# Kernel optimization log

Hardware: AMD Instinct MI355X
Metric: run time of the kernel (lower is better)

## Reference

```python
import jax, jax.numpy as jnp
import numpy as np

N_NODES = 100000
N_EDGES = 640000
D_IN = 128
D_H = 128


def setup_inputs() -> dict:
    key = jax.random.key(0)
    ks = jax.random.split(key, 24)
    def W(k, shp):
        return jax.random.normal(k, shp, dtype=jnp.float32) * 0.05
    inp = {
        "x": jax.random.normal(ks[0], (N_NODES, D_IN), dtype=jnp.float32),
        "src": jax.random.randint(ks[1], (N_EDGES,), 0, N_NODES, dtype=jnp.int32),
        "dst": jax.random.randint(ks[2], (N_EDGES,), 0, N_NODES, dtype=jnp.int32),
        "neg_src": jax.random.randint(ks[3], (N_EDGES,), 0, N_NODES, dtype=jnp.int32),
        "neg_dst": jax.random.randint(ks[4], (N_EDGES,), 0, N_NODES, dtype=jnp.int32),
        # SAGEConv layer 1/2/3: fc_self weight, fc_neigh weight (stored [in,out]), bias
        "Ws1": W(ks[5], (D_IN, D_H)), "Wn1": W(ks[6], (D_IN, D_H)), "b1": jnp.zeros((D_H,), jnp.float32),
        "Ws2": W(ks[7], (D_H, D_H)), "Wn2": W(ks[8], (D_H, D_H)), "b2": jnp.zeros((D_H,), jnp.float32),
        "Ws3": W(ks[9], (D_H, D_H)), "Wn3": W(ks[10], (D_H, D_H)), "b3": jnp.zeros((D_H,), jnp.float32),
        # MLPPredictor: W1 [2h,h], W2 [h,1]
        "Wp1": W(ks[11], (2 * D_H, D_H)), "bp1": jnp.zeros((D_H,), jnp.float32),
        "Wp2": W(ks[12], (D_H, 1)), "bp2": jnp.zeros((1,), jnp.float32),
    }
    return inp


def _sage_mean(x, src, dst, Ws, Wn, b):
    # DGL SAGEConv 'mean': rst = fc_self(h) + fc_neigh(mean_{in-neighbors}(h)) + bias
    n = x.shape[0]
    msum = jax.ops.segment_sum(x[src], dst, num_segments=n)        # [N, d]
    deg = jax.ops.segment_sum(jnp.ones_like(src, dtype=x.dtype), dst, num_segments=n)
    mean = msum / jnp.clip(deg, 1.0)[:, None]                      # zero for isolated nodes
    return x @ Ws + mean @ Wn + b


def _edge_score(h, s, d, Wp1, bp1, Wp2, bp2):
    z = jnp.concatenate([h[s], h[d]], axis=1)                      # [E, 2h]
    return (jax.nn.relu(z @ Wp1 + bp1) @ Wp2 + bp2)[:, 0]          # [E]


def reference(x, src, dst, neg_src, neg_dst,
              Ws1, Wn1, b1, Ws2, Wn2, b2, Ws3, Wn3, b3,
              Wp1, bp1, Wp2, bp2):
    h = _sage_mean(x, src, dst, Ws1, Wn1, b1)
    h = _sage_mean(h, src, dst, Ws2, Wn2, b2)
    h = _sage_mean(h, src, dst, Ws3, Wn3, b3)
    pos = _edge_score(h, src, dst, Wp1, bp1, Wp2, bp2)
    neg = _edge_score(h, neg_src, neg_dst, Wp1, bp1, Wp2, bp2)
    return (pos, neg)
```

## Files before the change

### kernel.cpp

```cpp
#include <hip/hip_runtime.h>

#define N_NODES 100000
#define N_EDGES 640000
#define D 128
#define SCAN_TILE 1024
#define SCAN_BLOCKS ((N_NODES + SCAN_TILE - 1) / SCAN_TILE)

typedef __attribute__((ext_vector_type(8))) short bf16x8;
typedef __attribute__((ext_vector_type(4))) float f32x4;

__device__ __forceinline__ unsigned short f32_to_bf16(float f) {
  union { float f; unsigned int u; } v; v.f = f;
  unsigned int u = v.u;
  unsigned int r = (u + 0x7fffu + ((u >> 16) & 1u)) >> 16;
  return (unsigned short)r;
}
__device__ __forceinline__ float bf16_lo(unsigned int u) { return __uint_as_float(u << 16); }
__device__ __forceinline__ float bf16_hi(unsigned int u) { return __uint_as_float(u & 0xffff0000u); }

__device__ __forceinline__ void acc8(float* a, uint4 r) {
  a[0] += bf16_lo(r.x); a[1] += bf16_hi(r.x);
  a[2] += bf16_lo(r.y); a[3] += bf16_hi(r.y);
  a[4] += bf16_lo(r.z); a[5] += bf16_hi(r.z);
  a[6] += bf16_lo(r.w); a[7] += bf16_hi(r.w);
}

__global__ void zero_i32(int* __restrict__ p, int n) {
  int i = blockIdx.x * blockDim.x + threadIdx.x;
  if (i < n) p[i] = 0;
}

__global__ void f32_to_bf16_vec(const float* __restrict__ in, unsigned short* __restrict__ out, int n4) {
  int i = blockIdx.x * blockDim.x + threadIdx.x;
  if (i < n4) {
    float4 v = ((const float4*)in)[i];
    ushort4 o;
    o.x = f32_to_bf16(v.x); o.y = f32_to_bf16(v.y);
    o.z = f32_to_bf16(v.z); o.w = f32_to_bf16(v.w);
    ((ushort4*)out)[i] = o;
  }
}

__global__ void transpose_w(const float* __restrict__ W0, const float* __restrict__ W1,
                            const float* __restrict__ W2, const float* __restrict__ W3,
                            const float* __restrict__ W4, const float* __restrict__ W5,
                            const float* __restrict__ W6, const float* __restrict__ W7,
                            unsigned short* __restrict__ wt) {
  int id = blockIdx.x * 256 + threadIdx.x;
  int mat = id >> 14;
  int rem = id & 16383;
  int n = rem >> 7, k = rem & 127;
  const float* Wm = mat < 4 ? (mat < 2 ? (mat == 0 ? W0 : W1) : (mat == 2 ? W2 : W3))
                            : (mat < 6 ? (mat == 4 ? W4 : W5) : (mat == 6 ? W6 : W7));
  wt[id] = f32_to_bf16(Wm[k * D + n]);
}

__global__ void hist_kernel(const int* __restrict__ dst, int* __restrict__ deg, int E) {
  int i = blockIdx.x * blockDim.x + threadIdx.x;
  if (i < E) atomicAdd(&deg[dst[i]], 1);
}

__global__ void scan_blocksum(const int* __restrict__ deg, int* __restrict__ partial, int n) {
  __shared__ int lds[256];
  const int tid = threadIdx.x;
  const int base = blockIdx.x * SCAN_TILE + tid * 4;
  int s = 0;
#pragma unroll
  for (int j = 0; j < 4; ++j) {
    int i = base + j;
    if (i < n) s += deg[i];
  }
  lds[tid] = s;
  __syncthreads();
  for (int off = 128; off > 0; off >>= 1) {
    if (tid < off) lds[tid] += lds[tid + off];
    __syncthreads();
  }
  if (tid == 0) partial[blockIdx.x] = lds[0];
}

__global__ void scan_offsets(int* __restrict__ partial, int* __restrict__ row_start, int nb, int n) {
  __shared__ int lds[128];
  const int tid = threadIdx.x;
  int v = (tid < nb) ? partial[tid] : 0;
  lds[tid] = v;
  __syncthreads();
  for (int off = 1; off < 128; off <<= 1) {
    int t = (tid >= off) ? lds[tid - off] : 0;
    __syncthreads();
    lds[tid] += t;
    __syncthreads();
  }
  if (tid < nb) partial[tid] = (tid == 0) ? 0 : lds[tid - 1];
  if (tid == 0) row_start[n] = lds[nb - 1];
}

__global__ void scan_final(const int* __restrict__ deg, const int* __restrict__ partial,
                           int* __restrict__ row_start, int n) {
  __shared__ int lds[256];
  const int tid = threadIdx.x;
  const int base = blockIdx.x * SCAN_TILE + tid * 4;
  int d[4];
  int s = 0;
#pragma unroll
  for (int j = 0; j < 4; ++j) {
    int i = base + j;
    d[j] = (i < n) ? deg[i] : 0;
    s += d[j];
  }
  lds[tid] = s;
  __syncthreads();
  for (int off = 1; off < 256; off <<= 1) {
    int t = (tid >= off) ? lds[tid - off] : 0;
    __syncthreads();
    lds[tid] += t;
    __syncthreads();
  }
  int pre = partial[blockIdx.x] + lds[tid] - s;
#pragma unroll
  for (int j = 0; j < 4; ++j) {
    int i = base + j;
    if (i < n) {
      row_start[i] = pre;
      pre += d[j];
    }
  }
}

__global__ void fill_kernel(const int* __restrict__ src, const int* __restrict__ dst,
                            const int* __restrict__ row_start, int* __restrict__ cursor,
                            int* __restrict__ esrc, int E) {
  int i = blockIdx.x * blockDim.x + threadIdx.x;
  if (i < E) {
    int d = dst[i];
    int pos = atomicAdd(&cursor[d], 1);
    esrc[row_start[d] + pos] = src[i];
  }
}

__global__ __launch_bounds__(256) void gather_mean(
    const unsigned short* __restrict__ hin,
    const int* __restrict__ row_start, const int* __restrict__ esrc,
    unsigned short* __restrict__ mean, int M) {
  const int t = blockIdx.x * blockDim.x + threadIdx.x;
  const int node = t >> 4;
  const int fl = t & 15;
  if (node >= M) return;
  const int s0 = row_start[node], s1 = row_start[node + 1];
  float ac[8] = {0.f, 0.f, 0.f, 0.f, 0.f, 0.f, 0.f, 0.f};
  int e = s0;
  for (; e + 4 <= s1; e += 4) {
    int i0 = esrc[e], i1 = esrc[e + 1], i2 = esrc[e + 2], i3 = esrc[e + 3];
    uint4 r0 = *(const uint4*)(hin + (((size_t)i0) << 7) + fl * 8);
    uint4 r1 = *(const uint4*)(hin + (((size_t)i1) << 7) + fl * 8);
    uint4 r2 = *(const uint4*)(hin + (((size_t)i2) << 7) + fl * 8);
    uint4 r3 = *(const uint4*)(hin + (((size_t)i3) << 7) + fl * 8);
    acc8(ac, r0); acc8(ac, r1); acc8(ac, r2); acc8(ac, r3);
  }
  for (; e < s1; ++e) {
    uint4 r0 = *(const uint4*)(hin + (((size_t)esrc[e]) << 7) + fl * 8);
    acc8(ac, r0);
  }
  const float inv = 1.0f / (float)max(s1 - s0, 1);
#pragma unroll
  for (int k = 0; k < 8; ++k) ac[k] *= inv;
  uint4 o;
  o.x = (unsigned)f32_to_bf16(ac[0]) | ((unsigned)f32_to_bf16(ac[1]) << 16);
  o.y = (unsigned)f32_to_bf16(ac[2]) | ((unsigned)f32_to_bf16(ac[3]) << 16);
  o.z = (unsigned)f32_to_bf16(ac[4]) | ((unsigned)f32_to_bf16(ac[5]) << 16);
  o.w = (unsigned)f32_to_bf16(ac[6]) | ((unsigned)f32_to_bf16(ac[7]) << 16);
  *reinterpret_cast<uint4*>(mean + (((size_t)node) << 7) + fl * 8) = o;
}

template <bool PRED>
__global__ __launch_bounds__(256) void layer_mlp(
    const unsigned short* __restrict__ hin,
    const unsigned short* __restrict__ mean,
    const unsigned short* __restrict__ Wts, const unsigned short* __restrict__ Wtn,
    const float* __restrict__ bias,
    const unsigned short* __restrict__ WtA, const unsigned short* __restrict__ WtB,
    const float* __restrict__ biasA,
    unsigned short* __restrict__ out0, unsigned short* __restrict__ out1, int M) {
  __shared__ unsigned short wl[64][136];
  __shared__ unsigned short mt[64][136];
  const int tid = threadIdx.x;
  const int lane = tid & 63;
  const int wave = tid >> 6;
  const int m0 = blockIdx.x * 64;
  const int row = lane & 15;
  const int q = lane >> 4;
  const int mw = m0 + wave * 16;
  const int mload = min(mw + row, M - 1);
  const int lrow = wave * 16 + row;

  auto stage64 = [&](const unsigned short* W, int half) {
#pragma unroll
    for (int i = 0; i < 4; ++i) {
      int seg = i * 256 + tid;
      int r = seg >> 4, o = (seg & 15) * 8;
      *reinterpret_cast<bf16x8*>(&wl[r][o]) =
          *reinterpret_cast<const bf16x8*>(W + (size_t)(half * 64 + r) * D + o);
    }
  };
  auto mfma_half = [&](bf16x8* a, f32x4* accp) {
#pragma unroll
    for (int s = 0; s < 4; ++s)
#pragma unroll
      for (int t = 0; t < 4; ++t) {
        bf16x8 b = *reinterpret_cast<const bf16x8*>(&wl[t * 16 + row][s * 32 + q * 8]);
        accp[t] = __builtin_amdgcn_mfma_f32_16x16x32_bf16(a[s], b, accp[t], 0, 0, 0);
      }
  };
  auto epilogue = [&](f32x4* accp, const float* bvec, unsigned short* dst) {
#pragma unroll
    for (int t = 0; t < 8; ++t) {
      const int col = t * 16 + row;
      const float bv = bvec ? bvec[col] : 0.f;
#pragma unroll
      for (int r = 0; r < 4; ++r)
        mt[wave * 16 + q * 4 + r][col] = f32_to_bf16(accp[t][r] + bv);
    }
    __syncthreads();
#pragma unroll
    for (int i = 0; i < 4; ++i) {
      int idx = i * 256 + tid;
      int r2 = idx >> 4;
      int c8 = (idx & 15) * 8;
      int m = m0 + r2;
      if (m < M)
        *reinterpret_cast<uint4*>(dst + (size_t)m * D + c8) =
            *reinterpret_cast<const uint4*>(&mt[r2][c8]);
    }
  };

  stage64(Wts, 0);
  bf16x8 ah[4], am[4];
#pragma unroll
  for (int s = 0; s < 4; ++s) {
    ah[s] = *reinterpret_cast<const bf16x8*>(hin + (size_t)mload * D + s * 32 + q * 8);
    am[s] = *reinterpret_cast<const bf16x8*>(mean + (size_t)mload * D + s * 32 + q * 8);
  }
  __syncthreads();

  f32x4 acc[8];
#pragma unroll
  for (int t = 0; t < 8; ++t) acc[t] = (f32x4){0.f, 0.f, 0.f, 0.f};

  mfma_half(ah, acc);
  __syncthreads(); stage64(Wts, 1); __syncthreads();
  mfma_half(ah, acc + 4);
  __syncthreads(); stage64(Wtn, 0); __syncthreads();
  mfma_half(am, acc);
  __syncthreads(); stage64(Wtn, 1); __syncthreads();
  mfma_half(am, acc + 4);

  if (!PRED) {
    epilogue(acc, bias, out0);
    return;
  }

  __syncthreads();
#pragma unroll
  for (int t = 0; t < 8; ++t) {
    const int col = t * 16 + row;
    const float bv = bias[col];
#pragma unroll
    for (int r = 0; r < 4; ++r)
      mt[wave * 16 + q * 4 + r][col] = f32_to_bf16(acc[t][r] + bv);
  }
  stage64(WtA, 0);
  __syncthreads();
  bf16x8 ap[4];
#pragma unroll
  for (int s = 0; s < 4; ++s)
    ap[s] = *reinterpret_cast<const bf16x8*>(&mt[lrow][s * 32 + q * 8]);

#pragma unroll
  for (int t = 0; t < 8; ++t) acc[t] = (f32x4){0.f, 0.f, 0.f, 0.f};
  mfma_half(ap, acc);
  __syncthreads(); stage64(WtA, 1); __syncthreads();
  mfma_half(ap, acc + 4);
  epilogue(acc, biasA, out0);
  __syncthreads(); stage64(WtB, 0); __syncthreads();
#pragma unroll
  for (int t = 0; t < 8; ++t) acc[t] = (f32x4){0.f, 0.f, 0.f, 0.f};
  mfma_half(ap, acc);
  __syncthreads(); stage64(WtB, 1); __syncthreads();
  mfma_half(ap, acc + 4);
  epilogue(acc, nullptr, out1);
}

__device__ __forceinline__ float relu_dot8(uint4 a, uint4 b, float4 w0, float4 w1) {
  return fmaxf(bf16_lo(a.x) + bf16_lo(b.x), 0.f) * w0.x +
         fmaxf(bf16_hi(a.x) + bf16_hi(b.x), 0.f) * w0.y +
         fmaxf(bf16_lo(a.y) + bf16_lo(b.y), 0.f) * w0.z +
         fmaxf(bf16_hi(a.y) + bf16_hi(b.y), 0.f) * w0.w +
         fmaxf(bf16_lo(a.z) + bf16_lo(b.z), 0.f) * w1.x +
         fmaxf(bf16_hi(a.z) + bf16_hi(b.z), 0.f) * w1.y +
         fmaxf(bf16_lo(a.w) + bf16_lo(b.w), 0.f) * w1.z +
         fmaxf(bf16_hi(a.w) + bf16_hi(b.w), 0.f) * w1.w;
}

__global__ __launch_bounds__(256) void edge_score4(
    const unsigned short* __restrict__ A, const unsigned short* __restrict__ B,
    const int* __restrict__ ss, const int* __restrict__ dd,
    const float* __restrict__ Wp2, const float* __restrict__ bp2,
    float* __restrict__ out, int E) {
  const int t = blockIdx.x * blockDim.x + threadIdx.x;
  const int g = t >> 4;
  const int fl = t & 15;
  const int e0 = g * 4;
  if (e0 >= E) return;
  const int4 s4 = *(const int4*)(ss + e0);
  const int4 d4 = *(const int4*)(dd + e0);
  const float4 w0 = *(const float4*)(Wp2 + fl * 8);
  const float4 w1 = *(const float4*)(Wp2 + fl * 8 + 4);
  const size_t fo = (size_t)(fl * 8);

  uint4 a0 = *(const uint4*)(A + (((size_t)s4.x << 7) + fo));
  uint4 b0 = *(const uint4*)(B + (((size_t)d4.x << 7) + fo));
  uint4 a1 = *(const uint4*)(A + (((size_t)s4.y << 7) + fo));
  uint4 b1 = *(const uint4*)(B + (((size_t)d4.y << 7) + fo));
  uint4 a2 = *(const uint4*)(A + (((size_t)s4.z << 7) + fo));
  uint4 b2 = *(const uint4*)(B + (((size_t)d4.z << 7) + fo));
  uint4 a3 = *(const uint4*)(A + (((size_t)s4.w << 7) + fo));
  uint4 b3 = *(const uint4*)(B + (((size_t)d4.w << 7) + fo));

  float p0 = relu_dot8(a0, b0, w0, w1);
  float p1 = relu_dot8(a1, b1, w0, w1);
  float p2 = relu_dot8(a2, b2, w0, w1);
  float p3 = relu_dot8(a3, b3, w0, w1);

  p0 += __shfl_xor(p0, 1); p1 += __shfl_xor(p1, 1); p2 += __shfl_xor(p2, 1); p3 += __shfl_xor(p3, 1);
  p0 += __shfl_xor(p0, 2); p1 += __shfl_xor(p1, 2); p2 += __shfl_xor(p2, 2); p3 += __shfl_xor(p3, 2);
  p0 += __shfl_xor(p0, 4); p1 += __shfl_xor(p1, 4); p2 += __shfl_xor(p2, 4); p3 += __shfl_xor(p3, 4);
  p0 += __shfl_xor(p0, 8); p1 += __shfl_xor(p1, 8); p2 += __shfl_xor(p2, 8); p3 += __shfl_xor(p3, 8);

  if (fl == 0) {
    const float bv = bp2[0];
    *reinterpret_cast<float4*>(out + e0) = make_float4(p0 + bv, p1 + bv, p2 + bv, p3 + bv);
  }
}

extern "C" void kernel_launch(void* const* d_in, const int* in_sizes, int n_in,
                              void* d_out, int out_size, void* d_ws, size_t ws_size,
                              hipStream_t stream) {
  const float* x = (const float*)d_in[0];
  const int* src = (const int*)d_in[1];
  const int* dst = (const int*)d_in[2];
  const int* nsrc = (const int*)d_in[3];
  const int* ndst = (const int*)d_in[4];
  const float* Ws1 = (const float*)d_in[5];
  const float* Wn1 = (const float*)d_in[6];
  const float* b1 = (const float*)d_in[7];
  const float* Ws2 = (const float*)d_in[8];
  const float* Wn2 = (const float*)d_in[9];
  const float* b2 = (const float*)d_in[10];
  const float* Ws3 = (const float*)d_in[11];
  const float* Wn3 = (const float*)d_in[12];
  const float* b3 = (const float*)d_in[13];
  const float* Wp1 = (const float*)d_in[14];
  const float* bp1 = (const float*)d_in[15];
  const float* Wp2 = (const float*)d_in[16];
  const float* bp2 = (const float*)d_in[17];
  float* out = (float*)d_out;

  char* ws = (char*)d_ws;
  size_t off = 0;
  auto alloc = [&](size_t bytes) -> void* {
    void* p = ws + off;
    off += (bytes + 255) & ~(size_t)255;
    return p;
  };
  const size_t NODE_F32 = sizeof(float) * (size_t)N_NODES * D;
  char* region0 = (char*)alloc(NODE_F32);
  char* region1 = (char*)alloc(NODE_F32);
  unsigned short* meanb = (unsigned short*)alloc(sizeof(unsigned short) * (size_t)N_NODES * D);
  int* row_start = (int*)alloc(sizeof(int) * (N_NODES + 1));
  int* deg = (int*)alloc(sizeof(int) * N_NODES * 2);
  int* cursor = deg + N_NODES;
  int* esrc = (int*)alloc(sizeof(int) * N_EDGES);
  int* partial = (int*)alloc(sizeof(int) * 128);
  unsigned short* wt = (unsigned short*)alloc(sizeof(unsigned short) * 8 * D * D);
  (void)ws_size;

  unsigned short* xb = (unsigned short*)region0;
  unsigned short* hA = (unsigned short*)region1;
  unsigned short* hB = hA + (size_t)N_NODES * D;
  unsigned short* Ab = xb;
  unsigned short* Bb = xb + (size_t)N_NODES * D;

  f32_to_bf16_vec<<<(N_NODES * D / 4 + 255) / 256, 256, 0, stream>>>(x, xb, N_NODES * D / 4);
  transpose_w<<<512, 256, 0, stream>>>(Ws1, Wn1, Ws2, Wn2, Ws3, Wn3, Wp1, Wp1 + D * D, wt);

  zero_i32<<<(2 * N_NODES + 255) / 256, 256, 0, stream>>>(deg, 2 * N_NODES);
  hist_kernel<<<(N_EDGES + 255) / 256, 256, 0, stream>>>(dst, deg, N_EDGES);
  scan_blocksum<<<SCAN_BLOCKS, 256, 0, stream>>>(deg, partial, N_NODES);
  scan_offsets<<<1, 128, 0, stream>>>(partial, row_start, SCAN_BLOCKS, N_NODES);
  scan_final<<<SCAN_BLOCKS, 256, 0, stream>>>(deg, partial, row_start, N_NODES);
  fill_kernel<<<(N_EDGES + 255) / 256, 256, 0, stream>>>(src, dst, row_start, cursor, esrc, N_EDGES);

  const int gatherBlocks = (N_NODES * 16 + 255) / 256;
  const int mlpBlocks = (N_NODES + 63) / 64;
  const int edgeBlocks = (N_EDGES / 4 * 16) / 256;

  gather_mean<<<gatherBlocks, 256, 0, stream>>>(xb, row_start, esrc, meanb, N_NODES);
  layer_mlp<false><<<mlpBlocks, 256, 0, stream>>>(
      xb, meanb, wt, wt + 16384, b1, nullptr, nullptr, nullptr, hA, nullptr, N_NODES);
  gather_mean<<<gatherBlocks, 256, 0, stream>>>(hA, row_start, esrc, meanb, N_NODES);
  layer_mlp<false><<<mlpBlocks, 256, 0, stream>>>(
      hA, meanb, wt + 2 * 16384, wt + 3 * 16384, b2, nullptr, nullptr, nullptr, hB, nullptr, N_NODES);
  gather_mean<<<gatherBlocks, 256, 0, stream>>>(hB, row_start, esrc, meanb, N_NODES);
  layer_mlp<true><<<mlpBlocks, 256, 0, stream>>>(
      hB, meanb, wt + 4 * 16384, wt + 5 * 16384, b3, wt + 6 * 16384, wt + 7 * 16384, bp1,
      Ab, Bb, N_NODES);
  edge_score4<<<edgeBlocks, 256, 0, stream>>>(Ab, Bb, src, dst, Wp2, bp2, out, N_EDGES);
  edge_score4<<<edgeBlocks, 256, 0, stream>>>(Ab, Bb, nsrc, ndst, Wp2, bp2, out + N_EDGES, N_EDGES);
}
```

Measured before the change: 457.0 us.

## Process 128 rows per MLP block to reuse staged weight tiles twice

Each layer_mlp block now handles two 64-row sub-tiles (A and B) against every staged 64-row weight half, halving the number of weight stagings to LDS per node and halving the block count. The separate output staging buffer is removed and the epilogue reuses the weight LDS buffer, with an extra barrier added. This doubles accumulator and A-operand register usage, which may reduce occupancy or cause spills.

```diff
diff --git a/kernel.cpp b/kernel.cpp
--- a/kernel.cpp
+++ b/kernel.cpp
@@ -182,15 +182,14 @@
     const float* __restrict__ biasA,
     unsigned short* __restrict__ out0, unsigned short* __restrict__ out1, int M) {
   __shared__ unsigned short wl[64][136];
-  __shared__ unsigned short mt[64][136];
   const int tid = threadIdx.x;
   const int lane = tid & 63;
   const int wave = tid >> 6;
-  const int m0 = blockIdx.x * 64;
+  const int m0 = blockIdx.x * 128;
   const int row = lane & 15;
   const int q = lane >> 4;
-  const int mw = m0 + wave * 16;
-  const int mload = min(mw + row, M - 1);
+  const int mloadA = min(m0 + wave * 16 + row, M - 1);
+  const int mloadB = min(m0 + 64 + wave * 16 + row, M - 1);
   const int lrow = wave * 16 + row;
 
   auto stage64 = [&](const unsigned short* W, int half) {
@@ -211,14 +210,15 @@
         accp[t] = __builtin_amdgcn_mfma_f32_16x16x32_bf16(a[s], b, accp[t], 0, 0, 0);
       }
   };
-  auto epilogue = [&](f32x4* accp, const float* bvec, unsigned short* dst) {
+  auto epilogue = [&](f32x4* accp, const float* bvec, unsigned short* dst, int base) {
+    __syncthreads();
 #pragma unroll
     for (int t = 0; t < 8; ++t) {
       const int col = t * 16 + row;
       const float bv = bvec ? bvec[col] : 0.f;
 #pragma unroll
       for (int r = 0; r < 4; ++r)
-        mt[wave * 16 + q * 4 + r][col] = f32_to_bf16(accp[t][r] + bv);
+        wl[wave * 16 + q * 4 + r][col] = f32_to_bf16(accp[t][r] + bv);
     }
     __syncthreads();
 #pragma unroll
@@ -226,68 +226,87 @@
       int idx = i * 256 + tid;
       int r2 = idx >> 4;
       int c8 = (idx & 15) * 8;
-      int m = m0 + r2;
+      int m = base + r2;
       if (m < M)
         *reinterpret_cast<uint4*>(dst + (size_t)m * D + c8) =
-            *reinterpret_cast<const uint4*>(&mt[r2][c8]);
+            *reinterpret_cast<const uint4*>(&wl[r2][c8]);
     }
   };
 
   stage64(Wts, 0);
-  bf16x8 ah[4], am[4];
+  bf16x8 ahA[4], amA[4], ahB[4], amB[4];
 #pragma unroll
   for (int s = 0; s < 4; ++s) {
-    ah[s] = *reinterpret_cast<const bf16x8*>(hin + (size_t)mload * D + s * 32 + q * 8);
-    am[s] = *reinterpret_cast<const bf16x8*>(mean + (size_t)mload * D + s * 32 + q * 8);
-  }
-  __syncthreads();
-
-  f32x4 acc[8];
-#pragma unroll
-  for (int t = 0; t < 8; ++t) acc[t] = (f32x4){0.f, 0.f, 0.f, 0.f};
-
-  mfma_half(ah, acc);
+    ahA[s] = *reinterpret_cast<const bf16x8*>(hin + (size_t)mloadA * D + s * 32 + q * 8);
+    amA[s] = *reinterpret_cast<const bf16x8*>(mean + (size_t)mloadA * D + s * 32 + q * 8);
+    ahB[s] = *reinterpret_cast<const bf16x8*>(hin + (size_t)mloadB * D + s * 32 + q * 8);
+    amB[s] = *reinterpret_cast<const bf16x8*>(mean + (size_t)mloadB * D + s * 32 + q * 8);
+  }
+  __syncthreads();
+
+  f32x4 accA[8], accB[8];
+#pragma unroll
+  for (int t = 0; t < 8; ++t) { accA[t] = (f32x4){0.f, 0.f, 0.f, 0.f}; accB[t] = (f32x4){0.f, 0.f, 0.f, 0.f}; }
+
+  mfma_half(ahA, accA); mfma_half(ahB, accB);
   __syncthreads(); stage64(Wts, 1); __syncthreads();
-  mfma_half(ah, acc + 4);
+  mfma_half(ahA, accA + 4); mfma_half(ahB, accB + 4);
   __syncthreads(); stage64(Wtn, 0); __syncthreads();
-  mfma_half(am, acc);
+  mfma_half(amA, accA); mfma_half(amB, accB);
   __syncthreads(); stage64(Wtn, 1); __syncthreads();
-  mfma_half(am, acc + 4);
+  mfma_half(amA, accA + 4); mfma_half(amB, accB + 4);
 
   if (!PRED) {
-    epilogue(acc, bias, out0);
+    epilogue(accA, bias, out0, m0);
+    epilogue(accB, bias, out0, m0 + 64);
     return;
   }
 
   __syncthreads();
+  bf16x8 apA[4], apB[4];
 #pragma unroll
   for (int t = 0; t < 8; ++t) {
     const int col = t * 16 + row;
     const float bv = bias[col];
 #pragma unroll
     for (int r = 0; r < 4; ++r)
-      mt[wave * 16 + q * 4 + r][col] = f32_to_bf16(acc[t][r] + bv);
-  }
+      wl[wave * 16 + q * 4 + r][col] = f32_to_bf16(accA[t][r] + bv);
+  }
+#pragma unroll
+  for (int s = 0; s < 4; ++s)
+    apA[s] = *reinterpret_cast<const bf16x8*>(&wl[lrow][s * 32 + q * 8]);
+#pragma unroll
+  for (int t = 0; t < 8; ++t) {
+    const int col = t * 16 + row;
+    const float bv = bias[col];
+#pragma unroll
+    for (int r = 0; r < 4; ++r)
+      wl[wave * 16 + q * 4 + r][col] = f32_to_bf16(accB[t][r] + bv);
+  }
+#pragma unroll
+  for (int s = 0; s < 4; ++s)
+    apB[s] = *reinterpret_cast<const bf16x8*>(&wl[lrow][s * 32 + q * 8]);
+  __syncthreads();
+
   stage64(WtA, 0);
   __syncthreads();
-  bf16x8 ap[4];
-#pragma unroll
-  for (int s = 0; s < 4; ++s)
-    ap[s] = *reinterpret_cast<const bf16x8*>(&mt[lrow][s * 32 + q * 8]);
-
-#pragma unroll
-  for (int t = 0; t < 8; ++t) acc[t] = (f32x4){0.f, 0.f, 0.f, 0.f};
-  mfma_half(ap, acc);
+#pragma unroll
+  for (int t = 0; t < 8; ++t) { accA[t] = (f32x4){0.f, 0.f, 0.f, 0.f}; accB[t] = (f32x4){0.f, 0.f, 0.f, 0.f}; }
+  mfma_half(apA, accA); mfma_half(apB, accB);
   __syncthreads(); stage64(WtA, 1); __syncthreads();
-  mfma_half(ap, acc + 4);
-  epilogue(acc, biasA, out0);
-  __syncthreads(); stage64(WtB, 0); __syncthreads();
-#pragma unroll
-  for (int t = 0; t < 8; ++t) acc[t] = (f32x4){0.f, 0.f, 0.f, 0.f};
-  mfma_half(ap, acc);
+  mfma_half(apA, accA + 4); mfma_half(apB, accB + 4);
+  epilogue(accA, biasA, out0, m0);
+  epilogue(accB, biasA, out0, m0 + 64);
+  __syncthreads();
+  stage64(WtB, 0);
+  __syncthreads();
+#pragma unroll
+  for (int t = 0; t < 8; ++t) { accA[t] = (f32x4){0.f, 0.f, 0.f, 0.f}; accB[t] = (f32x4){0.f, 0.f, 0.f, 0.f}; }
+  mfma_half(apA, accA); mfma_half(apB, accB);
   __syncthreads(); stage64(WtB, 1); __syncthreads();
-  mfma_half(ap, acc + 4);
-  epilogue(acc, nullptr, out1);
+  mfma_half(apA, accA + 4); mfma_half(apB, accB + 4);
+  epilogue(accA, nullptr, out1, m0);
+  epilogue(accB, nullptr, out1, m0 + 64);
 }
 
 __device__ __forceinline__ float relu_dot8(uint4 a, uint4 b, float4 w0, float4 w1) {
@@ -401,7 +420,7 @@
   fill_kernel<<<(N_EDGES + 255) / 256, 256, 0, stream>>>(src, dst, row_start, cursor, esrc, N_EDGES);
 
   const int gatherBlocks = (N_NODES * 16 + 255) / 256;
-  const int mlpBlocks = (N_NODES + 63) / 64;
+  const int mlpBlocks = (N_NODES + 127) / 128;
   const int edgeBlocks = (N_EDGES / 4 * 16) / 256;
 
   gather_mean<<<gatherBlocks, 256, 0, stream>>>(xb, row_start, esrc, meanb, N_NODES);
```

Measured after the change: 460.3 us. No clear change (+0.7%).
